# Kernel tuning notes

Measured on AMD Instinct MI355X. Metric: run time of the kernel, lower is better.

Reference implementation:

```python
import jax, jax.numpy as jnp
import numpy as np

B = 512            # graphs per batch
NV_PER, NA_PER = 40, 100
NV, NA = B * NV_PER, B * NA_PER      # 20480 video / 51200 audio nodes
EVV, EAA, EVA = NV * 8, NA * 8, NV * 3
DV, DA, H, OUT, L = 1024, 128, 512, 128, 4
EPS = 1e-5


def _gcn(x, W, b, src, dst, ew, n_dst):
    # GCNConv(normalize=False, add_self_loops=False) with edge weights:
    # out[d] = sum_{e: dst(e)=d} ew[e] * (x @ W)[src(e)] + b
    h = x @ W
    msg = h[src] * ew[:, None]
    return jax.ops.segment_sum(msg, dst, num_segments=n_dst) + b


def _gat(xs, xd, Ws, Wd, a_s, a_d, b, src, dst, n_dst):
    # GATConv-style bipartite attention, heads=1, concat=False, no self loops.
    hs = xs @ Ws                      # [Ns, H]
    hd = xd @ Wd                      # [Nd, H]
    logit = jax.nn.leaky_relu((hs @ a_s)[src] + (hd @ a_d)[dst], 0.2)  # [E]
    m = jax.ops.segment_max(logit, dst, num_segments=n_dst)
    m = jnp.where(jnp.isfinite(m), m, 0.0)          # guard empty segments
    e = jnp.exp(logit - m[dst])
    s = jax.ops.segment_sum(e, dst, num_segments=n_dst)
    alpha = e / s[dst]                               # softmax over incoming edges
    out = jax.ops.segment_sum(alpha[:, None] * hs[src], dst, num_segments=n_dst)
    return out + b


def _graph_norm(x, batch, w, bias):
    # PyG LayerNorm (graph mode): normalize over all nodes+channels per graph.
    C = x.shape[-1]
    cnt = jax.ops.segment_sum(jnp.ones((x.shape[0],), x.dtype), batch, num_segments=B)
    denom = jnp.maximum(cnt * C, 1.0)
    mean = jax.ops.segment_sum(x, batch, num_segments=B).sum(-1) / denom   # [B]
    xc = x - mean[batch][:, None]
    var = jax.ops.segment_sum(xc * xc, batch, num_segments=B).sum(-1) / denom
    return w * xc * jax.lax.rsqrt(var + EPS)[batch][:, None] + bias


def _readout(x, batch, att_w):
    # GlobalAttention: gate = softmax_per_graph(x @ att_w); out = sum gate*x
    g = x @ att_w                                    # [N]
    m = jax.ops.segment_max(g, batch, num_segments=B)
    m = jnp.where(jnp.isfinite(m), m, 0.0)
    e = jnp.exp(g - m[batch])
    s = jax.ops.segment_sum(e, batch, num_segments=B)
    alpha = e / jnp.maximum(s, 1e-16)[batch]
    return jax.ops.segment_sum(alpha[:, None] * x, batch, num_segments=B)  # [B, H]


def setup_inputs() -> dict:
    key = jax.random.key(0)
    ks = iter(jax.random.split(key, 40))

    def nrm(shape, scale=0.05):
        return scale * jax.random.normal(next(ks), shape, dtype=jnp.float32)

    inp = {
        'x_video': jax.random.normal(next(ks), (NV, DV), dtype=jnp.float32),
        'x_audio': jax.random.normal(next(ks), (NA, DA), dtype=jnp.float32),
        'ew_vv': jax.random.uniform(next(ks), (EVV,), dtype=jnp.float32),
        'ew_aa': jax.random.uniform(next(ks), (EAA,), dtype=jnp.float32),
        'W_vv0': nrm((DV, H)), 'W_aa0': nrm((DA, H)),
        'W_src0': nrm((DV, H)), 'W_dst0': nrm((DA, H)),
        'W_vv': nrm((L - 1, H, H)), 'W_aa': nrm((L - 1, H, H)),
        'W_src': nrm((L - 1, H, H)), 'W_dst': nrm((L - 1, H, H)),
        'b_vv': nrm((L, H)), 'b_aa': nrm((L, H)), 'b_gat': nrm((L, H)),
        'a_src': nrm((L, H)), 'a_dst': nrm((L, H)),
        'ln_v_w': jnp.ones((L, H), jnp.float32), 'ln_v_b': jnp.zeros((L, H), jnp.float32),
        'ln_a_w': jnp.ones((L, H), jnp.float32), 'ln_a_b': jnp.zeros((L, H), jnp.float32),
        'att_w': nrm((H,)), 'lin_W': nrm((H, OUT)), 'lin_b': nrm((OUT,)),
        'ei_vv': jax.random.randint(next(ks), (2, EVV), 0, NV, dtype=jnp.int32),
        'ei_aa': jax.random.randint(next(ks), (2, EAA), 0, NA, dtype=jnp.int32),
        'ei_va': jnp.stack([
            jax.random.randint(next(ks), (EVA,), 0, NV, dtype=jnp.int32),
            jax.random.randint(next(ks), (EVA,), 0, NA, dtype=jnp.int32)]),
        'batch_video': jnp.repeat(jnp.arange(B, dtype=jnp.int32), NV_PER),
        'batch_audio': jnp.repeat(jnp.arange(B, dtype=jnp.int32), NA_PER),
    }
    return inp


def reference(x_video, x_audio, ew_vv, ew_aa, W_vv0, W_aa0, W_src0, W_dst0,
              W_vv, W_aa, W_src, W_dst, b_vv, b_aa, b_gat, a_src, a_dst,
              ln_v_w, ln_v_b, ln_a_w, ln_a_b, att_w, lin_W, lin_b,
              ei_vv, ei_aa, ei_va, batch_video, batch_audio):
    xv, xa = x_video, x_audio
    for i in range(L):
        Wv = W_vv0 if i == 0 else W_vv[i - 1]
        Wa = W_aa0 if i == 0 else W_aa[i - 1]
        Ws = W_src0 if i == 0 else W_src[i - 1]
        Wd = W_dst0 if i == 0 else W_dst[i - 1]
        # HeteroConv(aggr='sum'): video <- vv GCN; audio <- aa GCN + va GAT
        nv = _gcn(xv, Wv, b_vv[i], ei_vv[0], ei_vv[1], ew_vv, NV)
        na = (_gcn(xa, Wa, b_aa[i], ei_aa[0], ei_aa[1], ew_aa, NA)
              + _gat(xv, xa, Ws, Wd, a_src[i], a_dst[i], b_gat[i],
                     ei_va[0], ei_va[1], NA))
        nv = jax.nn.relu(nv)
        na = jax.nn.relu(na)
        # (dropout p=0.1 omitted for deterministic reference)
        xv = _graph_norm(nv, batch_video, ln_v_w[i], ln_v_b[i])
        xa = _graph_norm(na, batch_audio, ln_a_w[i], ln_a_b[i])
    graph_embed = _readout(xa, batch_audio, att_w)   # [B, H]
    pred = graph_embed @ lin_W + lin_b               # [B, OUT]
    return pred
```

## Files before the change

kernel.cpp:

```cpp
#include <hip/hip_runtime.h>

#define NB   512
#define NV   20480
#define NA   51200
#define EVV  163840
#define EAA  409600
#define EVA  61440
#define DV   1024
#define DA   128
#define HD   512
#define NOUT 128
#define NL   4

#define VTILES 160
#define ATILES 400
#define GSEC0  (VTILES * 4)
#define GSEC1  (GSEC0 * 2)
#define GTOT   (GSEC1 + ATILES * 4)
#define ABLK   (NA / 4)
#define GBLK   ((NA + NV) / 4)

typedef __attribute__((ext_vector_type(8))) short short8;
typedef __attribute__((ext_vector_type(8))) unsigned short ushort8;
typedef __attribute__((ext_vector_type(4))) float f32x4;

__device__ inline unsigned short f2bf(float f) {
  unsigned u = __float_as_uint(f);
  return (unsigned short)((u + 0x7fffu + ((u >> 16) & 1u)) >> 16);
}
__device__ inline float bf2f(unsigned short h) {
  return __uint_as_float((unsigned)h << 16);
}

template <int AFF>
__global__ __launch_bounds__(256) void mfma_gemm3(const float* __restrict__ xv,
    const float* __restrict__ xa,
    const unsigned short* __restrict__ Wt_s, const unsigned short* __restrict__ Wt_v,
    const unsigned short* __restrict__ Wt_a,
    unsigned short* __restrict__ S_s, unsigned short* __restrict__ S_v,
    unsigned short* __restrict__ S_a, int Kv, int Ka,
    const float* __restrict__ mean_v, const float* __restrict__ rstd_v,
    const float* __restrict__ lnv_w, const float* __restrict__ lnv_b,
    const float* __restrict__ mean_a, const float* __restrict__ rstd_a,
    const float* __restrict__ lna_w, const float* __restrict__ lna_b) {
  __shared__ unsigned short As[128 * 40];
  __shared__ unsigned short Bs[128 * 40];
  const int id = blockIdx.x;
  const float* A; const unsigned short* Bt; unsigned short* C; int K; int lid;
  bool video;
  if (id < GSEC0)      { A = xv; Bt = Wt_s; C = S_s; K = Kv; lid = id; video = true; }
  else if (id < GSEC1) { A = xv; Bt = Wt_v; C = S_v; K = Kv; lid = id - GSEC0; video = true; }
  else                 { A = xa; Bt = Wt_a; C = S_a; K = Ka; lid = id - GSEC1; video = false; }
  const int xcd = lid & 7;
  const int j = lid >> 3;
  const int bn = j & 3;
  const int bm = xcd + ((j >> 2) << 3);
  const int tid = threadIdx.x;
  const int l = tid & 63, wid = tid >> 6;
  const int wr = wid >> 1, wc = wid & 1;
  const int r = tid >> 1;
  const int kh = (tid & 1) << 4;

  const float* ap = A + (size_t)(bm * 128 + r) * K + kh;
  const unsigned short* btp = Bt + (size_t)(bn * 128 + r) * K + kh;

  float mean = 0.f, rstd = 1.f;
  const float* lw = nullptr; const float* lb = nullptr;
  if (AFF) {
    int node = bm * 128 + r;
    int g = video ? node / 40 : node / 100;
    mean = video ? mean_v[g] : mean_a[g];
    rstd = video ? rstd_v[g] : rstd_a[g];
    lw = video ? lnv_w : lna_w;
    lb = video ? lnv_b : lna_b;
  }

  f32x4 acc[4][4] = {};
  const int fr = l & 15, fq = l >> 4;
  const int arow = (wr * 64 + fr) * 40 + fq * 8;
  const int brow = (wc * 64 + fr) * 40 + fq * 8;

  for (int k0 = 0; k0 < K; k0 += 32) {
    float4 f0 = *(const float4*)(ap + k0 + 0);
    float4 f1 = *(const float4*)(ap + k0 + 4);
    float4 f2 = *(const float4*)(ap + k0 + 8);
    float4 f3 = *(const float4*)(ap + k0 + 12);
    short8 bv0 = *(const short8*)(btp + k0);
    short8 bv1 = *(const short8*)(btp + k0 + 8);
    if (AFF) {
      const float* wp = lw + k0 + kh;
      const float* bp = lb + k0 + kh;
      float4 w0 = *(const float4*)(wp), w1 = *(const float4*)(wp + 4);
      float4 w2 = *(const float4*)(wp + 8), w3 = *(const float4*)(wp + 12);
      float4 c0 = *(const float4*)(bp), c1 = *(const float4*)(bp + 4);
      float4 c2 = *(const float4*)(bp + 8), c3 = *(const float4*)(bp + 12);
#define AFF1(v, w, c) v = w * (fmaxf(v, 0.f) - mean) * rstd + c;
      AFF1(f0.x, w0.x, c0.x) AFF1(f0.y, w0.y, c0.y) AFF1(f0.z, w0.z, c0.z) AFF1(f0.w, w0.w, c0.w)
      AFF1(f1.x, w1.x, c1.x) AFF1(f1.y, w1.y, c1.y) AFF1(f1.z, w1.z, c1.z) AFF1(f1.w, w1.w, c1.w)
      AFF1(f2.x, w2.x, c2.x) AFF1(f2.y, w2.y, c2.y) AFF1(f2.z, w2.z, c2.z) AFF1(f2.w, w2.w, c2.w)
      AFF1(f3.x, w3.x, c3.x) AFF1(f3.y, w3.y, c3.y) AFF1(f3.z, w3.z, c3.z) AFF1(f3.w, w3.w, c3.w)
#undef AFF1
    }
    short8 p0, p1;
    p0[0] = (short)f2bf(f0.x); p0[1] = (short)f2bf(f0.y);
    p0[2] = (short)f2bf(f0.z); p0[3] = (short)f2bf(f0.w);
    p0[4] = (short)f2bf(f1.x); p0[5] = (short)f2bf(f1.y);
    p0[6] = (short)f2bf(f1.z); p0[7] = (short)f2bf(f1.w);
    p1[0] = (short)f2bf(f2.x); p1[1] = (short)f2bf(f2.y);
    p1[2] = (short)f2bf(f2.z); p1[3] = (short)f2bf(f2.w);
    p1[4] = (short)f2bf(f3.x); p1[5] = (short)f2bf(f3.y);
    p1[6] = (short)f2bf(f3.z); p1[7] = (short)f2bf(f3.w);
    __syncthreads();
    *(short8*)&As[r * 40 + kh] = p0;
    *(short8*)&As[r * 40 + kh + 8] = p1;
    *(short8*)&Bs[r * 40 + kh] = bv0;
    *(short8*)&Bs[r * 40 + kh + 8] = bv1;
    __syncthreads();
    short8 a[4], b[4];
#pragma unroll
    for (int m = 0; m < 4; ++m) a[m] = *(const short8*)&As[arow + m * 16 * 40];
#pragma unroll
    for (int n = 0; n < 4; ++n) b[n] = *(const short8*)&Bs[brow + n * 16 * 40];
#pragma unroll
    for (int m = 0; m < 4; ++m)
#pragma unroll
      for (int n = 0; n < 4; ++n)
        acc[m][n] = __builtin_amdgcn_mfma_f32_16x16x32_bf16(a[m], b[n], acc[m][n], 0, 0, 0);
  }

#pragma unroll
  for (int m = 0; m < 4; ++m) {
#pragma unroll
    for (int n = 0; n < 4; ++n) {
      int col = bn * 128 + wc * 64 + n * 16 + fr;
#pragma unroll
      for (int j2 = 0; j2 < 4; ++j2) {
        int row = bm * 128 + wr * 64 + m * 16 + fq * 4 + j2;
        C[(size_t)row * HD + col] = f2bf(acc[m][n][j2]);
      }
    }
  }
}

__global__ __launch_bounds__(256) void tcast_kernel(const float* __restrict__ W,
    unsigned short* __restrict__ Wt, int K) {
  __shared__ float t[32][33];
  int n0 = blockIdx.x * 32, k0 = blockIdx.y * 32;
  int c = threadIdx.x & 31, rr = threadIdx.x >> 5;
#pragma unroll
  for (int i = 0; i < 4; ++i) {
    int row = rr + i * 8;
    t[row][c] = W[(size_t)(k0 + row) * HD + n0 + c];
  }
  __syncthreads();
#pragma unroll
  for (int i = 0; i < 4; ++i) {
    int row = rr + i * 8;
    Wt[(size_t)(n0 + row) * K + k0 + c] = f2bf(t[c][row]);
  }
}

__global__ __launch_bounds__(256) void gemm64(const float* __restrict__ A,
    const float* __restrict__ B, const float* __restrict__ bias,
    float* __restrict__ C, int M, int N, int K) {
  __shared__ float As[16][68];
  __shared__ float Bs[16][68];
  const int tid = threadIdx.x;
  const int bm = blockIdx.y, bn = blockIdx.x;
  const int tx = tid & 15, ty = tid >> 4;
  const int la_m = tid >> 2, la_k = (tid & 3) << 2;
  const int lb_k = tid >> 4, lb_n = (tid & 15) << 2;
  const float* Ab = A + (size_t)bm * 64 * K;
  const float* Bb = B + bn * 64;
  float acc[4][4] = {};
  for (int k0 = 0; k0 < K; k0 += 16) {
    float4 av = *(const float4*)(Ab + (size_t)la_m * K + k0 + la_k);
    float4 bv = *(const float4*)(Bb + (size_t)(k0 + lb_k) * N + lb_n);
    __syncthreads();
    As[la_k + 0][la_m] = av.x; As[la_k + 1][la_m] = av.y;
    As[la_k + 2][la_m] = av.z; As[la_k + 3][la_m] = av.w;
    *(float4*)&Bs[lb_k][lb_n] = bv;
    __syncthreads();
#pragma unroll
    for (int k = 0; k < 16; ++k) {
      float a0 = As[k][ty * 4 + 0], a1 = As[k][ty * 4 + 1];
      float a2 = As[k][ty * 4 + 2], a3 = As[k][ty * 4 + 3];
      float b0 = Bs[k][tx * 4 + 0], b1 = Bs[k][tx * 4 + 1];
      float b2 = Bs[k][tx * 4 + 2], b3 = Bs[k][tx * 4 + 3];
      acc[0][0] += a0 * b0; acc[0][1] += a0 * b1; acc[0][2] += a0 * b2; acc[0][3] += a0 * b3;
      acc[1][0] += a1 * b0; acc[1][1] += a1 * b1; acc[1][2] += a1 * b2; acc[1][3] += a1 * b3;
      acc[2][0] += a2 * b0; acc[2][1] += a2 * b1; acc[2][2] += a2 * b2; acc[2][3] += a2 * b3;
      acc[3][0] += a3 * b0; acc[3][1] += a3 * b1; acc[3][2] += a3 * b2; acc[3][3] += a3 * b3;
    }
  }
  const int col = bn * 64 + tx * 4;
  float4 bv = make_float4(0.f, 0.f, 0.f, 0.f);
  if (bias) bv = *(const float4*)(bias + col);
#pragma unroll
  for (int i = 0; i < 4; ++i) {
    size_t row = (size_t)bm * 64 + ty * 4 + i;
    float4 v = make_float4(acc[i][0] + bv.x, acc[i][1] + bv.y,
                           acc[i][2] + bv.z, acc[i][3] + bv.w);
    *(float4*)(C + row * N + col) = v;
  }
}

__global__ __launch_bounds__(256) void rowdot_kernel(const float* __restrict__ x,
    const float* __restrict__ w, float* __restrict__ out, int N, int K) {
  int row = blockIdx.x * 4 + (threadIdx.x >> 6);
  if (row >= N) return;
  int lane = threadIdx.x & 63;
  const float* xp = x + (size_t)row * K;
  float p = 0.f;
  for (int k = lane; k < K; k += 64) p += xp[k] * w[k];
  for (int off = 32; off; off >>= 1) p += __shfl_down(p, off);
  if (lane == 0) out[row] = p;
}

__global__ __launch_bounds__(256) void deg_kernel(const int* __restrict__ dst,
    int* __restrict__ deg, int E) {
  int e = blockIdx.x * 256 + threadIdx.x;
  if (e < E) atomicAdd(deg + dst[e], 1);
}

__global__ __launch_bounds__(256) void scan1_kernel(const int* __restrict__ deg,
    int* __restrict__ bsum, int n) {
  __shared__ int sh[4];
  int b = blockIdx.x, tid = threadIdx.x;
  int lane = tid & 63, wid = tid >> 6;
  int v = 0;
#pragma unroll
  for (int j = 0; j < 4; ++j) {
    int i = b * 1024 + j * 256 + tid;
    if (i < n) v += deg[i];
  }
  for (int off = 32; off; off >>= 1) v += __shfl_down(v, off);
  if (lane == 0) sh[wid] = v;
  __syncthreads();
  if (tid == 0) bsum[b] = sh[0] + sh[1] + sh[2] + sh[3];
}

__global__ __launch_bounds__(64) void scan2_kernel(int* __restrict__ bsum, int nb,
    int* __restrict__ rp_end) {
  int tid = threadIdx.x;
  int v = (tid < nb) ? bsum[tid] : 0;
  int x = v;
#pragma unroll
  for (int off = 1; off < 64; off <<= 1) {
    int y = __shfl_up(x, off);
    if (tid >= off) x += y;
  }
  if (tid < nb) bsum[tid] = x - v;
  if (tid == 63) *rp_end = x;
}

__global__ __launch_bounds__(256) void scan3_kernel(const int* __restrict__ deg,
    const int* __restrict__ bsum, int* __restrict__ rp, int n) {
  __shared__ int wsum[4];
  int b = blockIdx.x, tid = threadIdx.x;
  int lane = tid & 63, wid = tid >> 6;
  int carry = bsum[b];
#pragma unroll
  for (int c = 0; c < 4; ++c) {
    int i = b * 1024 + c * 256 + tid;
    int v = (i < n) ? deg[i] : 0;
    int x = v;
#pragma unroll
    for (int off = 1; off < 64; off <<= 1) {
      int y = __shfl_up(x, off);
      if (lane >= off) x += y;
    }
    if (lane == 63) wsum[wid] = x;
    __syncthreads();
    int woff = 0;
    for (int k = 0; k < wid; ++k) woff += wsum[k];
    if (i < n) rp[i] = carry + woff + x - v;
    carry += wsum[0] + wsum[1] + wsum[2] + wsum[3];
    __syncthreads();
  }
}

__global__ __launch_bounds__(256) void copy_kernel(const int* __restrict__ a,
    int* __restrict__ b, int n) {
  int i = blockIdx.x * 256 + threadIdx.x;
  if (i < n) b[i] = a[i];
}

__global__ __launch_bounds__(256) void fill_kernel(const int* __restrict__ dst,
    int* __restrict__ cursor, int* __restrict__ eidx, int E) {
  int e = blockIdx.x * 256 + threadIdx.x;
  if (e >= E) return;
  int pos = atomicAdd(cursor + dst[e], 1);
  eidx[pos] = e;
}

__global__ __launch_bounds__(512) void uvec_kernel(const float* __restrict__ wsa_all,
    const float* __restrict__ wda_all,
    const float* __restrict__ ln_v_w, const float* __restrict__ ln_v_b,
    const float* __restrict__ ln_a_w, const float* __restrict__ ln_a_b,
    float* __restrict__ u_v, float* __restrict__ u_a, float* __restrict__ cc) {
  int b = blockIdx.x, tr = b >> 1, side = b & 1;
  int c = threadIdx.x;
  const float* d  = side ? wda_all + (tr + 1) * 512 : wsa_all + (tr + 1) * 1024;
  const float* lw = side ? ln_a_w + tr * HD : ln_v_w + tr * HD;
  const float* lb = side ? ln_a_b + tr * HD : ln_v_b + tr * HD;
  float dv = d[c];
  float uu = lw[c] * dv;
  float bv = lb[c] * dv;
  (side ? u_a : u_v)[tr * 512 + c] = uu;
  for (int off = 32; off; off >>= 1) { uu += __shfl_down(uu, off); bv += __shfl_down(bv, off); }
  __shared__ float s1[8], s2[8];
  int lane = c & 63, wid = c >> 6;
  if (lane == 0) { s1[wid] = uu; s2[wid] = bv; }
  __syncthreads();
  if (c == 0) {
    float a = 0, bb = 0;
    for (int i = 0; i < 8; ++i) { a += s1[i]; bb += s2[i]; }
    cc[tr * 4 + side * 2] = a;
    cc[tr * 4 + side * 2 + 1] = bb;
  }
}

__global__ __launch_bounds__(256) void initab_kernel(float* __restrict__ Av,
    float* __restrict__ Bv, float* __restrict__ Aa, float* __restrict__ Ba) {
  int i = blockIdx.x * 256 + threadIdx.x;
  if (i < NB) { Av[i] = 1.f; Bv[i] = 0.f; Aa[i] = 1.f; Ba[i] = 0.f; }
}

__device__ inline void acc_edges(const unsigned short* __restrict__ h,
    const int* __restrict__ rp, const int* __restrict__ eidx,
    const int* __restrict__ esrc, const float* __restrict__ ew,
    int d, int lane, float4& a0, float4& a1) {
  int beg = rp[d], end = rp[d + 1];
  for (int base = beg; base < end; base += 64) {
    int cnt = end - base; if (cnt > 64) cnt = 64;
    int s = 0; float w = 0.f;
    if (lane < cnt) {
      int e = eidx[base + lane];
      s = esrc[e];
      w = ew[e];
    }
    for (int j = 0; j < cnt; ++j) {
      int sj = __shfl(s, j);
      float wj = __shfl(w, j);
      ushort8 hv = *(const ushort8*)(h + (size_t)sj * HD + lane * 8);
      a0.x += wj * bf2f(hv[0]); a0.y += wj * bf2f(hv[1]);
      a0.z += wj * bf2f(hv[2]); a0.w += wj * bf2f(hv[3]);
      a1.x += wj * bf2f(hv[4]); a1.y += wj * bf2f(hv[5]);
      a1.z += wj * bf2f(hv[6]); a1.w += wj * bf2f(hv[7]);
    }
  }
}

__global__ __launch_bounds__(256) void gather_all(
    const unsigned short* __restrict__ S_a, const unsigned short* __restrict__ S_s,
    const unsigned short* __restrict__ S_v,
    const int* __restrict__ rp_aa, const int* __restrict__ ex_aa, const int* __restrict__ ei_aa,
    const float* __restrict__ ew_aa,
    const int* __restrict__ rp_va, const int* __restrict__ ex_va, const int* __restrict__ ei_va,
    const int* __restrict__ rp_vv, const int* __restrict__ ex_vv, const int* __restrict__ ei_vv,
    const float* __restrict__ ew_vv,
    const float* __restrict__ b_aa, const float* __restrict__ b_gat,
    const float* __restrict__ b_vv,
    const float* __restrict__ tv_cur, const float* __restrict__ ta_cur,
    const float* __restrict__ Av, const float* __restrict__ Bv,
    const float* __restrict__ Aa, const float* __restrict__ Ba,
    const float* __restrict__ u_v, const float* __restrict__ u_a,
    float* __restrict__ tv_next, float* __restrict__ ta_next,
    float* __restrict__ Q, float* __restrict__ P,
    float* __restrict__ psum, float* __restrict__ psq, int cdots) {
  int blk = blockIdx.x;
  int wv = threadIdx.x >> 6;
  int idx = blk * 4 + wv;
  int lane = threadIdx.x & 63;
  float4 a0, a1;
  bool audio = idx < NA;
  if (audio) {
    a0 = *(const float4*)(b_aa + lane * 8);
    a1 = *(const float4*)(b_aa + lane * 8 + 4);
    float4 c0 = *(const float4*)(b_gat + lane * 8);
    float4 c1 = *(const float4*)(b_gat + lane * 8 + 4);
    a0.x += c0.x; a0.y += c0.y; a0.z += c0.z; a0.w += c0.w;
    a1.x += c1.x; a1.y += c1.y; a1.z += c1.z; a1.w += c1.w;
    acc_edges(S_a, rp_aa, ex_aa, ei_aa, ew_aa, idx, lane, a0, a1);
    int beg = rp_va[idx], end = rp_va[idx + 1];
    if (end > beg) {
      int gd = idx / 100;
      float ld = Aa[gd] * ta_cur[idx] + Ba[gd];
      float ssum = 0.f;
      for (int base = beg; base < end; base += 64) {
        int cnt = end - base; if (cnt > 64) cnt = 64;
        float ex = 0.f;
        if (lane < cnt) {
          int e = ex_va[base + lane];
          int s = ei_va[e];
          int gs = s / 40;
          float l = Av[gs] * tv_cur[s] + Bv[gs] + ld;
          l = (l > 0.f) ? l : 0.2f * l;
          ex = __expf(l);
        }
        float t = ex;
        for (int off = 32; off; off >>= 1) t += __shfl_down(t, off);
        ssum += __shfl(t, 0);
      }
      float inv = 1.f / ssum;
      for (int base = beg; base < end; base += 64) {
        int cnt = end - base; if (cnt > 64) cnt = 64;
        int s = 0; float ex = 0.f;
        if (lane < cnt) {
          int e = ex_va[base + lane];
          s = ei_va[e];
          int gs = s / 40;
          float l = Av[gs] * tv_cur[s] + Bv[gs] + ld;
          l = (l > 0.f) ? l : 0.2f * l;
          ex = __expf(l);
        }
        for (int j = 0; j < cnt; ++j) {
          int sj = __shfl(s, j);
          float wj = __shfl(ex, j) * inv;
          ushort8 hv = *(const ushort8*)(S_s + (size_t)sj * HD + lane * 8);
          a0.x += wj * bf2f(hv[0]); a0.y += wj * bf2f(hv[1]);
          a0.z += wj * bf2f(hv[2]); a0.w += wj * bf2f(hv[3]);
          a1.x += wj * bf2f(hv[4]); a1.y += wj * bf2f(hv[5]);
          a1.z += wj * bf2f(hv[6]); a1.w += wj * bf2f(hv[7]);
        }
      }
    }
    float* op = Q + (size_t)idx * HD + lane * 8;
    *(float4*)(op) = a0;
    *(float4*)(op + 4) = a1;
  } else {
    int d = idx - NA;
    a0 = *(const float4*)(b_vv + lane * 8);
    a1 = *(const float4*)(b_vv + lane * 8 + 4);
    acc_edges(S_v, rp_vv, ex_vv, ei_vv, ew_vv, d, lane, a0, a1);
    float* op = P + (size_t)d * HD + lane * 8;
    *(float4*)(op) = a0;
    *(float4*)(op + 4) = a1;
  }
  float rs = 0.f, rq = 0.f;
#define RELQ(x) { float v_ = fmaxf(x, 0.f); rs += v_; rq += v_ * v_; }
  RELQ(a0.x) RELQ(a0.y) RELQ(a0.z) RELQ(a0.w)
  RELQ(a1.x) RELQ(a1.y) RELQ(a1.z) RELQ(a1.w)
#undef RELQ
  float rs2 = rs, rq2 = rq;
  for (int off = 32; off; off >>= 1) {
    rs2 += __shfl_down(rs2, off);
    rq2 += __shfl_down(rq2, off);
  }
  __shared__ float bs[4], bq[4];
  if (lane == 0) { bs[wv] = rs2; bq[wv] = rq2; }
  if (cdots) {
    const float* u = audio ? u_a : u_v;
    float4 u0 = *(const float4*)(u + lane * 8);
    float4 u1 = *(const float4*)(u + lane * 8 + 4);
    float tn = u0.x * fmaxf(a0.x, 0.f) + u0.y * fmaxf(a0.y, 0.f)
             + u0.z * fmaxf(a0.z, 0.f) + u0.w * fmaxf(a0.w, 0.f)
             + u1.x * fmaxf(a1.x, 0.f) + u1.y * fmaxf(a1.y, 0.f)
             + u1.z * fmaxf(a1.z, 0.f) + u1.w * fmaxf(a1.w, 0.f);
    for (int off = 32; off; off >>= 1) tn += __shfl_down(tn, off);
    if (lane == 0) {
      if (audio) ta_next[idx] = tn;
      else       tv_next[idx - NA] = tn;
    }
  }
  __syncthreads();
  if (threadIdx.x == 0) {
    psum[blk] = bs[0] + bs[1] + bs[2] + bs[3];
    psq[blk]  = bq[0] + bq[1] + bq[2] + bq[3];
  }
}

__global__ __launch_bounds__(256) void finalize_kernel(const float* __restrict__ psum,
    const float* __restrict__ psq,
    float* __restrict__ mean_a, float* __restrict__ rstd_a,
    float* __restrict__ mean_v, float* __restrict__ rstd_v,
    float* __restrict__ Aa, float* __restrict__ Ba,
    float* __restrict__ Av, float* __restrict__ Bv,
    const float* __restrict__ cc, int tr, int wnext) {
  int i = blockIdx.x * 256 + threadIdx.x;
  if (i >= 2 * NB) return;
  bool aud = i < NB;
  int g = aud ? i : i - NB;
  int pbase = aud ? g * 25 : ABLK + g * 10;
  int pcnt = aud ? 25 : 10;
  float s = 0.f, q = 0.f;
  for (int k = 0; k < pcnt; ++k) { s += psum[pbase + k]; q += psq[pbase + k]; }
  float M = aud ? 100.f * 512.f : 40.f * 512.f;
  float mean = s / M;
  float var = q / M - mean * mean;
  float rstd = rsqrtf(fmaxf(var, 0.f) + 1e-5f);
  if (aud) { mean_a[g] = mean; rstd_a[g] = rstd; }
  else     { mean_v[g] = mean; rstd_v[g] = rstd; }
  if (wnext) {
    float c1 = cc[tr * 4 + (aud ? 2 : 0)];
    float c2 = cc[tr * 4 + (aud ? 2 : 0) + 1];
    float A = rstd, B = -rstd * mean * c1 + c2;
    if (aud) { Aa[g] = A; Ba[g] = B; }
    else     { Av[g] = A; Bv[g] = B; }
  }
}

__global__ __launch_bounds__(512) void readout_kernel(const float* __restrict__ xa,
    const float* __restrict__ att_w,
    const float* __restrict__ mean_a, const float* __restrict__ rstd_a,
    const float* __restrict__ lw, const float* __restrict__ lb,
    float* __restrict__ ge) {
  int g = blockIdx.x;
  int tid = threadIdx.x;
  int lane = tid & 63, wid = tid >> 6;
  const float* xg = xa + (size_t)g * 100 * HD;
  float mean = mean_a[g], rstd = rstd_a[g];
  __shared__ float gv[112];
  for (int n = wid; n < 100; n += 8) {
    float p = 0.f;
#pragma unroll
    for (int j = 0; j < 8; ++j) {
      int c = j * 64 + lane;
      float o = lw[c] * (fmaxf(xg[(size_t)n * HD + c], 0.f) - mean) * rstd + lb[c];
      p += o * att_w[c];
    }
    for (int off = 32; off; off >>= 1) p += __shfl_down(p, off);
    if (lane == 0) gv[n] = p;
  }
  __syncthreads();
  __shared__ float inv_s;
  if (tid == 0) {
    float m = -1e30f;
    for (int n = 0; n < 100; ++n) m = fmaxf(m, gv[n]);
    float ssum = 0.f;
    for (int n = 0; n < 100; ++n) { float e = __expf(gv[n] - m); gv[n] = e; ssum += e; }
    inv_s = 1.0f / fmaxf(ssum, 1e-16f);
  }
  __syncthreads();
  float inv = inv_s;
  float wwc = lw[tid], bbc = lb[tid];
  float acc = 0.f;
  for (int n = 0; n < 100; ++n) {
    float o = wwc * (fmaxf(xg[(size_t)n * HD + tid], 0.f) - mean) * rstd + bbc;
    acc += gv[n] * o;
  }
  ge[(size_t)g * HD + tid] = acc * inv;
}

extern "C" void kernel_launch(void* const* d_in, const int* in_sizes, int n_in,
                              void* d_out, int out_size, void* d_ws, size_t ws_size,
                              hipStream_t stream) {
  const float* x_video = (const float*)d_in[0];
  const float* x_audio = (const float*)d_in[1];
  const float* ew_vv   = (const float*)d_in[2];
  const float* ew_aa   = (const float*)d_in[3];
  const float* W_vv0   = (const float*)d_in[4];
  const float* W_aa0   = (const float*)d_in[5];
  const float* W_src0  = (const float*)d_in[6];
  const float* W_dst0  = (const float*)d_in[7];
  const float* W_vv    = (const float*)d_in[8];
  const float* W_aa    = (const float*)d_in[9];
  const float* W_src   = (const float*)d_in[10];
  const float* W_dst   = (const float*)d_in[11];
  const float* b_vv    = (const float*)d_in[12];
  const float* b_aa    = (const float*)d_in[13];
  const float* b_gat   = (const float*)d_in[14];
  const float* a_src   = (const float*)d_in[15];
  const float* a_dst   = (const float*)d_in[16];
  const float* ln_v_w  = (const float*)d_in[17];
  const float* ln_v_b  = (const float*)d_in[18];
  const float* ln_a_w  = (const float*)d_in[19];
  const float* ln_a_b  = (const float*)d_in[20];
  const float* att_w   = (const float*)d_in[21];
  const float* lin_W   = (const float*)d_in[22];
  const float* lin_b   = (const float*)d_in[23];
  const int*   ei_vv   = (const int*)d_in[24];
  const int*   ei_aa   = (const int*)d_in[25];
  const int*   ei_va   = (const int*)d_in[26];

  const size_t WT_ELEMS = (size_t)HD * DV;
  const size_t REQ = (size_t)NV * HD + (size_t)NA * HD
                   + (size_t)NA * HD / 2 + (size_t)NV * HD
                   + 2 * NV + 2 * NA + 4096 + 2048 + 3 * 512 * 2 + 16
                   + 8 * NB + 2 * GBLK + (size_t)NB * HD
                   + (NV + 1) + EVV + (NA + 1) + EAA + (NA + 1) + EVA
                   + 3 * (WT_ELEMS / 2) + 64;
  if (ws_size < REQ * sizeof(float)) return;

  float* p = (float*)d_ws;
  float* P  = p; p += (size_t)NV * HD;
  float* Q  = p; p += (size_t)NA * HD;
  unsigned short* S_a = (unsigned short*)p; p += (size_t)NA * HD / 2;
  unsigned short* S_s = (unsigned short*)p; p += (size_t)NV * HD / 2;
  unsigned short* S_v = (unsigned short*)p; p += (size_t)NV * HD / 2;
  float* tv0 = p; p += NV;
  float* tv1 = p; p += NV;
  float* ta0 = p; p += NA;
  float* ta1 = p; p += NA;
  float* wsa_all = p; p += 4096;
  float* wda_all = p; p += 2048;
  float* u_v = p; p += 3 * 512;
  float* u_a = p; p += 3 * 512;
  float* cc  = p; p += 16;
  float* mean_a = p; p += NB;
  float* rstd_a = p; p += NB;
  float* mean_v = p; p += NB;
  float* rstd_v = p; p += NB;
  float* Aa = p; p += NB;
  float* Ba = p; p += NB;
  float* Av = p; p += NB;
  float* Bv = p; p += NB;
  float* psum = p; p += GBLK;
  float* psq  = p; p += GBLK;
  float* ge   = p; p += (size_t)NB * HD;
  int* rp_vv = (int*)p; p += NV + 1;
  int* ex_vv = (int*)p; p += EVV;
  int* rp_aa = (int*)p; p += NA + 1;
  int* ex_aa = (int*)p; p += EAA;
  int* rp_va = (int*)p; p += NA + 1;
  int* ex_va = (int*)p; p += EVA;
  unsigned short* Wt_v = (unsigned short*)p; p += WT_ELEMS / 2;
  unsigned short* Wt_a = (unsigned short*)p; p += WT_ELEMS / 2;
  unsigned short* Wt_s = (unsigned short*)p; p += WT_ELEMS / 2;
  int* bsum = (int*)p; p += 64;

  int* degbuf = (int*)ta0;
  int* curbuf = (int*)ta1;

  {
    struct { const int* dst; int* rp; int* ex; int N; int E; } g[3] = {
      { ei_vv + EVV, rp_vv, ex_vv, NV, EVV },
      { ei_aa + EAA, rp_aa, ex_aa, NA, EAA },
      { ei_va + EVA, rp_va, ex_va, NA, EVA },
    };
    for (int i = 0; i < 3; ++i) {
      int nb = (g[i].N + 1023) / 1024;
      hipMemsetAsync(degbuf, 0, (size_t)g[i].N * sizeof(int), stream);
      deg_kernel<<<(g[i].E + 255) / 256, 256, 0, stream>>>(g[i].dst, degbuf, g[i].E);
      scan1_kernel<<<nb, 256, 0, stream>>>(degbuf, bsum, g[i].N);
      scan2_kernel<<<1, 64, 0, stream>>>(bsum, nb, g[i].rp + g[i].N);
      scan3_kernel<<<nb, 256, 0, stream>>>(degbuf, bsum, g[i].rp, g[i].N);
      copy_kernel<<<(g[i].N + 255) / 256, 256, 0, stream>>>(g[i].rp, curbuf, g[i].N);
      fill_kernel<<<(g[i].E + 255) / 256, 256, 0, stream>>>(g[i].dst, curbuf, g[i].ex, g[i].E);
    }
  }

  for (int i = 0; i < NL; ++i) {
    const int Kv = (i == 0) ? DV : HD;
    const int Ka = (i == 0) ? DA : HD;
    const float* Ws = (i == 0) ? W_src0 : W_src + (size_t)(i - 1) * HD * HD;
    const float* Wd = (i == 0) ? W_dst0 : W_dst + (size_t)(i - 1) * HD * HD;
    rowdot_kernel<<<(Ka + 3) / 4, 256, 0, stream>>>(Wd, a_dst + i * HD, wda_all + i * 512, Ka, HD);
    rowdot_kernel<<<(Kv + 3) / 4, 256, 0, stream>>>(Ws, a_src + i * HD, wsa_all + i * 1024, Kv, HD);
  }
  rowdot_kernel<<<NA / 4, 256, 0, stream>>>(x_audio, wda_all, ta0, NA, DA);
  rowdot_kernel<<<NV / 4, 256, 0, stream>>>(x_video, wsa_all, tv0, NV, DV);
  uvec_kernel<<<6, 512, 0, stream>>>(wsa_all, wda_all, ln_v_w, ln_v_b, ln_a_w, ln_a_b,
                                     u_v, u_a, cc);
  initab_kernel<<<(NB + 255) / 256, 256, 0, stream>>>(Av, Bv, Aa, Ba);

  const float* xv_cur = x_video;
  const float* xa_cur = x_audio;
  float* tv_cur = tv0; float* tv_nxt = tv1;
  float* ta_cur = ta0; float* ta_nxt = ta1;

  for (int i = 0; i < NL; ++i) {
    const int Kv = (i == 0) ? DV : HD;
    const int Ka = (i == 0) ? DA : HD;
    const float* Wv = (i == 0) ? W_vv0  : W_vv  + (size_t)(i - 1) * HD * HD;
    const float* Wa = (i == 0) ? W_aa0  : W_aa  + (size_t)(i - 1) * HD * HD;
    const float* Ws = (i == 0) ? W_src0 : W_src + (size_t)(i - 1) * HD * HD;

    tcast_kernel<<<dim3(HD / 32, Kv / 32), 256, 0, stream>>>(Wv, Wt_v, Kv);
    tcast_kernel<<<dim3(HD / 32, Ka / 32), 256, 0, stream>>>(Wa, Wt_a, Ka);
    tcast_kernel<<<dim3(HD / 32, Kv / 32), 256, 0, stream>>>(Ws, Wt_s, Kv);

    if (i == 0)
      mfma_gemm3<0><<<GTOT, 256, 0, stream>>>(xv_cur, xa_cur, Wt_s, Wt_v, Wt_a,
          S_s, S_v, S_a, Kv, Ka,
          nullptr, nullptr, nullptr, nullptr, nullptr, nullptr, nullptr, nullptr);
    else
      mfma_gemm3<1><<<GTOT, 256, 0, stream>>>(xv_cur, xa_cur, Wt_s, Wt_v, Wt_a,
          S_s, S_v, S_a, Kv, Ka,
          mean_v, rstd_v, ln_v_w + (i - 1) * HD, ln_v_b + (i - 1) * HD,
          mean_a, rstd_a, ln_a_w + (i - 1) * HD, ln_a_b + (i - 1) * HD);

    int cdots = (i + 1 < NL) ? 1 : 0;
    gather_all<<<GBLK, 256, 0, stream>>>(S_a, S_s, S_v,
        rp_aa, ex_aa, ei_aa, ew_aa, rp_va, ex_va, ei_va,
        rp_vv, ex_vv, ei_vv, ew_vv,
        b_aa + i * HD, b_gat + i * HD, b_vv + i * HD,
        tv_cur, ta_cur, Av, Bv, Aa, Ba,
        u_v + i * 512, u_a + i * 512,
        tv_nxt, ta_nxt, Q, P, psum, psq, cdots);

    finalize_kernel<<<(2 * NB + 255) / 256, 256, 0, stream>>>(psum, psq,
        mean_a, rstd_a, mean_v, rstd_v, Aa, Ba, Av, Bv, cc, i, cdots);

    xv_cur = P;
    xa_cur = Q;
    float* t;
    t = tv_cur; tv_cur = tv_nxt; tv_nxt = t;
    t = ta_cur; ta_cur = ta_nxt; ta_nxt = t;
  }

  readout_kernel<<<NB, 512, 0, stream>>>(Q, att_w, mean_a, rstd_a,
      ln_a_w + (NL - 1) * HD, ln_a_b + (NL - 1) * HD, ge);
  gemm64<<<dim3(NOUT / 64, NB / 64), 256, 0, stream>>>(ge, lin_W, lin_b, (float*)d_out, NB, NOUT, HD);
}
```

Measured before the change: 1.356 ms.

## Fold graph-norm affine into weights and GEMM epilogue instead of A-tile prologue

Instead of applying the per-node LayerNorm affine (w*(relu(x)-mean)*rstd+b) to every A element inside the GEMM k-loop, the LN weight is folded into the transposed bf16 weights during tcast. Per-graph mean/rstd and the bias term are applied in the epilogue using precomputed column sums of the scaled weights and of the bias-weighted weights. The k-loop now only does ReLU and bf16 conversion, removing the per-iteration LN parameter loads and FMAs. This adds small colsum kernels and changes rounding order, since mean subtraction now happens after the bf16 GEMM, which could cause cancellation error.

Result: slower. 1.521 ms (+12.2%).

```diff
diff --git a/kernel.cpp b/kernel.cpp
--- a/kernel.cpp
+++ b/kernel.cpp
@@ -40,17 +40,17 @@
     unsigned short* __restrict__ S_s, unsigned short* __restrict__ S_v,
     unsigned short* __restrict__ S_a, int Kv, int Ka,
     const float* __restrict__ mean_v, const float* __restrict__ rstd_v,
-    const float* __restrict__ lnv_w, const float* __restrict__ lnv_b,
     const float* __restrict__ mean_a, const float* __restrict__ rstd_a,
-    const float* __restrict__ lna_w, const float* __restrict__ lna_b) {
+    const float* __restrict__ st_s, const float* __restrict__ st_v,
+    const float* __restrict__ st_a) {
   __shared__ unsigned short As[128 * 40];
   __shared__ unsigned short Bs[128 * 40];
   const int id = blockIdx.x;
   const float* A; const unsigned short* Bt; unsigned short* C; int K; int lid;
-  bool video;
-  if (id < GSEC0)      { A = xv; Bt = Wt_s; C = S_s; K = Kv; lid = id; video = true; }
-  else if (id < GSEC1) { A = xv; Bt = Wt_v; C = S_v; K = Kv; lid = id - GSEC0; video = true; }
-  else                 { A = xa; Bt = Wt_a; C = S_a; K = Ka; lid = id - GSEC1; video = false; }
+  const float* stp; bool video;
+  if (id < GSEC0)      { A = xv; Bt = Wt_s; C = S_s; K = Kv; lid = id; stp = st_s; video = true; }
+  else if (id < GSEC1) { A = xv; Bt = Wt_v; C = S_v; K = Kv; lid = id - GSEC0; stp = st_v; video = true; }
+  else                 { A = xa; Bt = Wt_a; C = S_a; K = Ka; lid = id - GSEC1; stp = st_a; video = false; }
   const int xcd = lid & 7;
   const int j = lid >> 3;
   const int bn = j & 3;
@@ -64,17 +64,6 @@
   const float* ap = A + (size_t)(bm * 128 + r) * K + kh;
   const unsigned short* btp = Bt + (size_t)(bn * 128 + r) * K + kh;
 
-  float mean = 0.f, rstd = 1.f;
-  const float* lw = nullptr; const float* lb = nullptr;
-  if (AFF) {
-    int node = bm * 128 + r;
-    int g = video ? node / 40 : node / 100;
-    mean = video ? mean_v[g] : mean_a[g];
-    rstd = video ? rstd_v[g] : rstd_a[g];
-    lw = video ? lnv_w : lna_w;
-    lb = video ? lnv_b : lna_b;
-  }
-
   f32x4 acc[4][4] = {};
   const int fr = l & 15, fq = l >> 4;
   const int arow = (wr * 64 + fr) * 40 + fq * 8;
@@ -88,18 +77,14 @@
     short8 bv0 = *(const short8*)(btp + k0);
     short8 bv1 = *(const short8*)(btp + k0 + 8);
     if (AFF) {
-      const float* wp = lw + k0 + kh;
-      const float* bp = lb + k0 + kh;
-      float4 w0 = *(const float4*)(wp), w1 = *(const float4*)(wp + 4);
-      float4 w2 = *(const float4*)(wp + 8), w3 = *(const float4*)(wp + 12);
-      float4 c0 = *(const float4*)(bp), c1 = *(const float4*)(bp + 4);
-      float4 c2 = *(const float4*)(bp + 8), c3 = *(const float4*)(bp + 12);
-#define AFF1(v, w, c) v = w * (fmaxf(v, 0.f) - mean) * rstd + c;
-      AFF1(f0.x, w0.x, c0.x) AFF1(f0.y, w0.y, c0.y) AFF1(f0.z, w0.z, c0.z) AFF1(f0.w, w0.w, c0.w)
-      AFF1(f1.x, w1.x, c1.x) AFF1(f1.y, w1.y, c1.y) AFF1(f1.z, w1.z, c1.z) AFF1(f1.w, w1.w, c1.w)
-      AFF1(f2.x, w2.x, c2.x) AFF1(f2.y, w2.y, c2.y) AFF1(f2.z, w2.z, c2.z) AFF1(f2.w, w2.w, c2.w)
-      AFF1(f3.x, w3.x, c3.x) AFF1(f3.y, w3.y, c3.y) AFF1(f3.z, w3.z, c3.z) AFF1(f3.w, w3.w, c3.w)
-#undef AFF1
+      f0.x = fmaxf(f0.x, 0.f); f0.y = fmaxf(f0.y, 0.f);
+      f0.z = fmaxf(f0.z, 0.f); f0.w = fmaxf(f0.w, 0.f);
+      f1.x = fmaxf(f1.x, 0.f); f1.y = fmaxf(f1.y, 0.f);
+      f1.z = fmaxf(f1.z, 0.f); f1.w = fmaxf(f1.w, 0.f);
+      f2.x = fmaxf(f2.x, 0.f); f2.y = fmaxf(f2.y, 0.f);
+      f2.z = fmaxf(f2.z, 0.f); f2.w = fmaxf(f2.w, 0.f);
+      f3.x = fmaxf(f3.x, 0.f); f3.y = fmaxf(f3.y, 0.f);
+      f3.z = fmaxf(f3.z, 0.f); f3.w = fmaxf(f3.w, 0.f);
     }
     short8 p0, p1;
     p0[0] = (short)f2bf(f0.x); p0[1] = (short)f2bf(f0.y);
@@ -130,20 +115,36 @@
 
 #pragma unroll
   for (int m = 0; m < 4; ++m) {
+    float rs4[4], rm4[4];
+    if (AFF) {
+#pragma unroll
+      for (int j2 = 0; j2 < 4; ++j2) {
+        int row = bm * 128 + wr * 64 + m * 16 + fq * 4 + j2;
+        int g = video ? row / 40 : row / 100;
+        float rs_ = video ? rstd_v[g] : rstd_a[g];
+        float mn_ = video ? mean_v[g] : mean_a[g];
+        rs4[j2] = rs_;
+        rm4[j2] = rs_ * mn_;
+      }
+    }
 #pragma unroll
     for (int n = 0; n < 4; ++n) {
       int col = bn * 128 + wc * 64 + n * 16 + fr;
+      float s_c = 0.f, t_c = 0.f;
+      if (AFF) { s_c = stp[col]; t_c = stp[512 + col]; }
 #pragma unroll
       for (int j2 = 0; j2 < 4; ++j2) {
         int row = bm * 128 + wr * 64 + m * 16 + fq * 4 + j2;
-        C[(size_t)row * HD + col] = f2bf(acc[m][n][j2]);
+        float val = acc[m][n][j2];
+        if (AFF) val = rs4[j2] * val - rm4[j2] * s_c + t_c;
+        C[(size_t)row * HD + col] = f2bf(val);
       }
     }
   }
 }
 
 __global__ __launch_bounds__(256) void tcast_kernel(const float* __restrict__ W,
-    unsigned short* __restrict__ Wt, int K) {
+    const float* __restrict__ ln, unsigned short* __restrict__ Wt, int K) {
   __shared__ float t[32][33];
   int n0 = blockIdx.x * 32, k0 = blockIdx.y * 32;
   int c = threadIdx.x & 31, rr = threadIdx.x >> 5;
@@ -153,10 +154,31 @@
     t[row][c] = W[(size_t)(k0 + row) * HD + n0 + c];
   }
   __syncthreads();
+  float lf = ln ? ln[k0 + c] : 1.0f;
 #pragma unroll
   for (int i = 0; i < 4; ++i) {
     int row = rr + i * 8;
-    Wt[(size_t)(n0 + row) * K + k0 + c] = f2bf(t[c][row]);
+    Wt[(size_t)(n0 + row) * K + k0 + c] = f2bf(lf * t[c][row]);
+  }
+}
+
+__global__ __launch_bounds__(512) void colsum_kernel(const float* __restrict__ W,
+    const float* __restrict__ lnw, const float* __restrict__ lnb,
+    float* __restrict__ st) {
+  int c = threadIdx.x & 63, kq = threadIdx.x >> 6;
+  int n = blockIdx.x * 64 + c;
+  float s = 0.f, t = 0.f;
+  for (int k = kq * 64; k < kq * 64 + 64; ++k) {
+    float w = W[(size_t)k * HD + n];
+    s += bf2f(f2bf(lnw[k] * w));
+    t += lnb[k] * w;
+  }
+  __shared__ float sr[8][64], tr_[8][64];
+  sr[kq][c] = s; tr_[kq][c] = t;
+  __syncthreads();
+  if (kq == 0) {
+    for (int q = 1; q < 8; ++q) { s += sr[q][c]; t += tr_[q][c]; }
+    st[n] = s; st[512 + n] = t;
   }
 }
 
@@ -578,7 +600,7 @@
   const size_t REQ = (size_t)NV * HD + (size_t)NA * HD
                    + (size_t)NA * HD / 2 + (size_t)NV * HD
                    + 2 * NV + 2 * NA + 4096 + 2048 + 3 * 512 * 2 + 16
-                   + 8 * NB + 2 * GBLK + (size_t)NB * HD
+                   + 8 * NB + 2 * GBLK + (size_t)NB * HD + 9 * 1024
                    + (NV + 1) + EVV + (NA + 1) + EAA + (NA + 1) + EVA
                    + 3 * (WT_ELEMS / 2) + 64;
   if (ws_size < REQ * sizeof(float)) return;
@@ -609,6 +631,7 @@
   float* psum = p; p += GBLK;
   float* psq  = p; p += GBLK;
   float* ge   = p; p += (size_t)NB * HD;
+  float* st_all = p; p += 9 * 1024;
   int* rp_vv = (int*)p; p += NV + 1;
   int* ex_vv = (int*)p; p += EVV;
   int* rp_aa = (int*)p; p += NA + 1;
@@ -654,6 +677,13 @@
   uvec_kernel<<<6, 512, 0, stream>>>(wsa_all, wda_all, ln_v_w, ln_v_b, ln_a_w, ln_a_b,
                                      u_v, u_a, cc);
   initab_kernel<<<(NB + 255) / 256, 256, 0, stream>>>(Av, Bv, Aa, Ba);
+  for (int tr = 0; tr < 3; ++tr) {
+    const float* lvw = ln_v_w + tr * HD; const float* lvb = ln_v_b + tr * HD;
+    const float* law = ln_a_w + tr * HD; const float* lab = ln_a_b + tr * HD;
+    colsum_kernel<<<8, 512, 0, stream>>>(W_src + (size_t)tr * HD * HD, lvw, lvb, st_all + (tr * 3 + 0) * 1024);
+    colsum_kernel<<<8, 512, 0, stream>>>(W_vv  + (size_t)tr * HD * HD, lvw, lvb, st_all + (tr * 3 + 1) * 1024);
+    colsum_kernel<<<8, 512, 0, stream>>>(W_aa  + (size_t)tr * HD * HD, law, lab, st_all + (tr * 3 + 2) * 1024);
+  }
 
   const float* xv_cur = x_video;
   const float* xa_cur = x_audio;
@@ -666,20 +696,24 @@
     const float* Wv = (i == 0) ? W_vv0  : W_vv  + (size_t)(i - 1) * HD * HD;
     const float* Wa = (i == 0) ? W_aa0  : W_aa  + (size_t)(i - 1) * HD * HD;
     const float* Ws = (i == 0) ? W_src0 : W_src + (size_t)(i - 1) * HD * HD;
-
-    tcast_kernel<<<dim3(HD / 32, Kv / 32), 256, 0, stream>>>(Wv, Wt_v, Kv);
-    tcast_kernel<<<dim3(HD / 32, Ka / 32), 256, 0, stream>>>(Wa, Wt_a, Ka);
-    tcast_kernel<<<dim3(HD / 32, Kv / 32), 256, 0, stream>>>(Ws, Wt_s, Kv);
+    const float* lnv_prev = (i == 0) ? nullptr : ln_v_w + (size_t)(i - 1) * HD;
+    const float* lna_prev = (i == 0) ? nullptr : ln_a_w + (size_t)(i - 1) * HD;
+
+    tcast_kernel<<<dim3(HD / 32, Kv / 32), 256, 0, stream>>>(Wv, lnv_prev, Wt_v, Kv);
+    tcast_kernel<<<dim3(HD / 32, Ka / 32), 256, 0, stream>>>(Wa, lna_prev, Wt_a, Ka);
+    tcast_kernel<<<dim3(HD / 32, Kv / 32), 256, 0, stream>>>(Ws, lnv_prev, Wt_s, Kv);
 
     if (i == 0)
       mfma_gemm3<0><<<GTOT, 256, 0, stream>>>(xv_cur, xa_cur, Wt_s, Wt_v, Wt_a,
           S_s, S_v, S_a, Kv, Ka,
-          nullptr, nullptr, nullptr, nullptr, nullptr, nullptr, nullptr, nullptr);
-    else
+          nullptr, nullptr, nullptr, nullptr, nullptr, nullptr, nullptr);
+    else {
+      const float* stb = st_all + (size_t)(i - 1) * 3 * 1024;
       mfma_gemm3<1><<<GTOT, 256, 0, stream>>>(xv_cur, xa_cur, Wt_s, Wt_v, Wt_a,
           S_s, S_v, S_a, Kv, Ka,
-          mean_v, rstd_v, ln_v_w + (i - 1) * HD, ln_v_b + (i - 1) * HD,
-          mean_a, rstd_a, ln_a_w + (i - 1) * HD, ln_a_b + (i - 1) * HD);
+          mean_v, rstd_v, mean_a, rstd_a,
+          stb, stb + 1024, stb + 2048);
+    }
 
     int cdots = (i + 1 < NL) ? 1 : 0;
     gather_all<<<GBLK, 256, 0, stream>>>(S_a, S_s, S_v,
```
